# Performance work log

Hardware: AMD Instinct MI355X
Metric: run time of the kernel (lower is better)

The kernel has to match this reference:

```python
import jax, jax.numpy as jnp
import numpy as np

HEAD_SIZE = 64
N_EMBED = 1024

def setup_inputs() -> dict:
    key = jax.random.key(0)
    kx, kk, kq, kv = jax.random.split(key, 4)
    x = jax.random.normal(kx, (8, 2048, N_EMBED), dtype=jnp.float32)
    # torch nn.Linear weights: [out_features, in_features]
    s = 1.0 / np.sqrt(N_EMBED)
    Wk = jax.random.uniform(kk, (HEAD_SIZE, N_EMBED), jnp.float32, -s, s)
    Wq = jax.random.uniform(kq, (HEAD_SIZE, N_EMBED), jnp.float32, -s, s)
    Wv = jax.random.uniform(kv, (HEAD_SIZE, N_EMBED), jnp.float32, -s, s)
    return {"x": x, "Wk": Wk, "Wq": Wq, "Wv": Wv}

def reference(x, Wk, Wq, Wv):
    B, T, C = x.shape
    k = x @ Wk.T  # [B,T,H]
    q = x @ Wq.T
    v = x @ Wv.T
    # NOTE: original computes k @ q^T and scales by sqrt(C)=sqrt(n_embed)
    wei = jnp.einsum('btd,bsd->bts', k, q) / jnp.sqrt(jnp.float32(C))
    mask = jnp.tril(jnp.ones((T, T), dtype=bool))
    wei = jnp.where(mask, wei, -jnp.inf)
    wei = jax.nn.softmax(wei, axis=-1)
    return wei @ v  # [B,T,H]
```

## Files before the change

kernel.cpp:

```cpp
#include <hip/hip_runtime.h>
#include <hip/hip_bf16.h>


typedef __attribute__((ext_vector_type(8))) short short8;
typedef __attribute__((ext_vector_type(4))) float f32x4;
typedef __attribute__((ext_vector_type(16))) float f32x16;
typedef unsigned int u32;

#define BATCH 8
#define T 2048
#define CDIM 1024
#define HD 64
#define QK_SCALE 0.04508422f

static __device__ __forceinline__ short f2bf(float f) {
    return __builtin_bit_cast(short, __float2bfloat16(f));
}
static __device__ __forceinline__ float bf2f(unsigned short s) {
    u32 u = ((u32)s) << 16;
    return __builtin_bit_cast(float, u);
}
static __device__ __forceinline__ u32 packbf(float lo, float hi) {
    return (u32)(unsigned short)f2bf(lo) | ((u32)(unsigned short)f2bf(hi) << 16);
}
static __device__ __forceinline__ f32x4 mfma16(short8 a, short8 b, f32x4 c) {
    return __builtin_amdgcn_mfma_f32_16x16x32_bf16(a, b, c, 0, 0, 0);
}
static __device__ __forceinline__ f32x16 mfma32(short8 a, short8 b, f32x16 c) {
    return __builtin_amdgcn_mfma_f32_32x32x16_bf16(a, b, c, 0, 0, 0);
}

#define SOFT_BARRIER { \
    __builtin_amdgcn_sched_barrier(0); \
    asm volatile("s_waitcnt lgkmcnt(0)" ::: "memory"); \
    __builtin_amdgcn_s_barrier(); \
    __builtin_amdgcn_sched_barrier(0); }

__global__ __launch_bounds__(256) void wcvt_kernel(
    const float* __restrict__ Wk, const float* __restrict__ Wq,
    const float* __restrict__ Wv, short* __restrict__ wfrag)
{
    const int t = blockIdx.x * 256 + threadIdx.x;
    const int lane = t & 63, kk = (t >> 6) & 31, d16 = (t >> 11) & 3, p = t >> 13;
    const float* __restrict__ W = (p == 0) ? Wk : (p == 1 ? Wq : Wv);
    const float sc = (p == 0) ? QK_SCALE : 1.0f;
    const float* src = W + (size_t)(d16 * 16 + (lane & 15)) * CDIM
                         + kk * 32 + ((lane >> 4) & 3) * 8;
    f32x4 a = *(const f32x4*)src;
    f32x4 b = *(const f32x4*)(src + 4);
    short8 o;
#pragma unroll
    for (int e = 0; e < 4; ++e) { o[e] = f2bf(a[e] * sc); o[e + 4] = f2bf(b[e] * sc); }
    *(short8*)(wfrag + (size_t)t * 8) = o;
}

#define XLOAD(KC) { \
    xr0 = *(const f32x4*)(xsrc + (KC) * 64); \
    xr1 = *(const f32x4*)(xsrc + (KC) * 64 + 4); }

#define XWRITE(BASE) { \
    short8 v = { f2bf(xr0[0]), f2bf(xr0[1]), f2bf(xr0[2]), f2bf(xr0[3]), \
                 f2bf(xr1[0]), f2bf(xr1[1]), f2bf(xr1[2]), f2bf(xr1[3]) }; \
    *(short8*)((BASE) + srow * 128 + ((sseg * 16) ^ ((srow & 7) << 4))) = v; }

#define BLOAD(DST, KC) \
    _Pragma("unroll") for (int u = 0; u < 6; ++u) \
        DST[u] = *(const short8*)&wfrag[(size_t)((cg * 3 + (u % 3)) * 32 + (KC) * 2 + (u / 3)) * 512 + lane * 8];

#define COMPUTE(XBASE, B) \
    _Pragma("unroll") for (int kkL = 0; kkL < 2; ++kkL) { \
        short8 af0 = *(short8*)((XBASE) + c * 128 + ((kkL * 64 + g * 16) ^ ((c & 7) << 4))); \
        short8 af1 = *(short8*)((XBASE) + (16 + c) * 128 + ((kkL * 64 + g * 16) ^ ((c & 7) << 4))); \
        _Pragma("unroll") for (int j = 0; j < 3; ++j) { \
            acc[0][j] = mfma16(af0, B[kkL * 3 + j], acc[0][j]); \
            acc[1][j] = mfma16(af1, B[kkL * 3 + j], acc[1][j]); } }

__global__ __launch_bounds__(256) void proj_kernel(
    const float* __restrict__ x, const short* __restrict__ wfrag,
    short* __restrict__ kfrag, short* __restrict__ qfrag, short* __restrict__ vfrag)
{
    __shared__ __align__(16) char lds[16384];

    const int tid = threadIdx.x, cg = tid >> 6, lane = tid & 63;
    const int c = lane & 15, g = lane >> 4;
    const int srow = tid >> 3, sseg = tid & 7;
    const int row0 = blockIdx.x * 32;
    const float* __restrict__ xsrc = x + (size_t)(row0 + srow) * CDIM + sseg * 8;

    f32x4 acc[2][3] = {};
    short8 bC[6], bN[6];
    f32x4 xr0, xr1;

    XLOAD(0)
    XWRITE(lds)
    XLOAD(1)
    BLOAD(bC, 0)
    __syncthreads();

#pragma unroll
    for (int k = 0; k < 16; ++k) {
        char* pc = lds + (k % 3) * 4096;
        char* pw = lds + ((k + 1) % 3) * 4096;
        if (k < 15) { XWRITE(pw) }
        if (k < 14) { XLOAD(k + 2) }
        if (k < 15) { BLOAD(bN, k + 1) }
        COMPUTE(pc, bC)
        SOFT_BARRIER
        if (k < 15) {
#pragma unroll
            for (int u = 0; u < 6; ++u) bC[u] = bN[u];
        }
    }

    short* st_k = (short*)lds;
    short* st_q = (short*)(lds + 4608);
    short* st_v = (short*)(lds + 9216);
#pragma unroll
    for (int j = 0; j < 3; ++j) {
        const int q = cg * 3 + j, p = q >> 2, d16 = q & 3;
#pragma unroll
        for (int rh = 0; rh < 2; ++rh)
#pragma unroll
            for (int r = 0; r < 4; ++r) {
                const int mrow = rh * 16 + g * 4 + r;
                const short v = f2bf(acc[rh][j][r]);
                if (p == 0)      st_k[mrow * 72 + d16 * 16 + c] = v;
                else if (p == 1) st_q[mrow * 72 + d16 * 16 + c] = v;
                else             st_v[(d16 * 16 + c) * 40 + mrow] = v;
            }
    }
    __syncthreads();

    const int b = row0 >> 11, i = (row0 & 2047) >> 5;
    const size_t tb = ((size_t)(b * 64 + i)) * 4;
    const int l5 = lane & 31, h = lane >> 5;
    const int fq = cg;

    short8 kv = *(short8*)&st_k[l5 * 72 + fq * 16 + h * 8];
    *(short8*)&kfrag[(tb + fq) * 512 + lane * 8] = kv;
    short8 qv = *(short8*)&st_q[l5 * 72 + fq * 16 + h * 8];
    *(short8*)&qfrag[(tb + fq) * 512 + lane * 8] = qv;
    const int dh = fq >> 1, ssub = fq & 1;
    short8 vv = *(short8*)&st_v[(dh * 32 + l5) * 40 + ssub * 16 + h * 8];
    *(short8*)&vfrag[(tb + fq) * 512 + lane * 8] = vv;
}

__global__ __launch_bounds__(512) void attn_kernel(
    const short* __restrict__ kfrag, const short* __restrict__ qfrag,
    const short* __restrict__ vfrag, float* __restrict__ out)
{
    const int tid = threadIdx.x, wid = tid >> 6, lane = tid & 63;
    const int l5 = lane & 31, h = lane >> 5;
    const int bx = blockIdx.x;
    const int i = 63 - (bx >> 3);
    const int b = bx & 7;
    const int t0 = i * 32;

    __shared__ u32   sO[8][32][32];
    __shared__ float sML[8][2][32];

    const short* __restrict__ kb = kfrag + ((size_t)(b * 64 + i)) * 2048;
    const short* __restrict__ qb = qfrag + ((size_t)b * 64) * 2048;
    const short* __restrict__ vb = vfrag + ((size_t)b * 64) * 2048;

    short8 kf[4];
#pragma unroll
    for (int ks = 0; ks < 4; ++ks)
        kf[ks] = *(const short8*)&kb[ks * 512 + lane * 8];

    float m = -1e30f, l = 0.f;
    f32x16 o0 = {}, o1 = {};

    short8 qf[4], vf[4], qn[4], vn[4];
#pragma unroll
    for (int ks = 0; ks < 4; ++ks) {
        qf[ks] = *(const short8*)&qb[((size_t)wid * 4 + ks) * 512 + lane * 8];
        vf[ks] = *(const short8*)&vb[((size_t)wid * 4 + ks) * 512 + lane * 8];
    }

    for (int st = wid; st <= i; st += 8) {
        f32x16 Cs = {};
#pragma unroll
        for (int ks = 0; ks < 4; ++ks)
            Cs = mfma32(qf[ks], kf[ks], Cs);

        if (st + 8 <= i) {
#pragma unroll
            for (int ks = 0; ks < 4; ++ks) {
                qn[ks] = *(const short8*)&qb[((size_t)(st + 8) * 4 + ks) * 512 + lane * 8];
                vn[ks] = *(const short8*)&vb[((size_t)(st + 8) * 4 + ks) * 512 + lane * 8];
            }
        }

        if (st == i) {
#pragma unroll
            for (int r = 0; r < 16; ++r) {
                const int srow = (r & 3) + 8 * (r >> 2) + 4 * h;
                if (srow > l5) Cs[r] = -1e30f;
            }
        }
        float mx = fmaxf(Cs[0], Cs[1]);
#pragma unroll
        for (int r = 2; r < 16; ++r) mx = fmaxf(mx, Cs[r]);
        mx = fmaxf(mx, __shfl_xor(mx, 32));
        if (!__all(mx <= m)) {
            const float mnew = fmaxf(m, mx);
            const float alpha = exp2f(m - mnew);
            m = mnew;
            l *= alpha;
#pragma unroll
            for (int r = 0; r < 16; ++r) { o0[r] *= alpha; o1[r] *= alpha; }
        }
        u32 pk[8];
        float rs = 0.f;
#pragma unroll
        for (int q = 0; q < 8; ++q) {
            const float e0 = exp2f(Cs[2 * q] - m);
            const float e1 = exp2f(Cs[2 * q + 1] - m);
            rs += e0 + e1;
            pk[q] = packbf(e0, e1);
        }
        rs += __shfl_xor(rs, 32);
        l += rs;

        u32 w0 = pk[0], w2 = pk[2];
        asm volatile("v_permlane32_swap_b32 %0, %1" : "+v"(w0), "+v"(w2));
        u32 w1 = pk[1], w3 = pk[3];
        asm volatile("v_permlane32_swap_b32 %0, %1" : "+v"(w1), "+v"(w3));
        u32 w4 = pk[4], w6 = pk[6];
        asm volatile("v_permlane32_swap_b32 %0, %1" : "+v"(w4), "+v"(w6));
        u32 w5 = pk[5], w7 = pk[7];
        asm volatile("v_permlane32_swap_b32 %0, %1" : "+v"(w5), "+v"(w7));
        short8 pf0, pf1;
        pf0[0] = (short)(w0 & 0xffff); pf0[1] = (short)(w0 >> 16);
        pf0[2] = (short)(w1 & 0xffff); pf0[3] = (short)(w1 >> 16);
        pf0[4] = (short)(w2 & 0xffff); pf0[5] = (short)(w2 >> 16);
        pf0[6] = (short)(w3 & 0xffff); pf0[7] = (short)(w3 >> 16);
        pf1[0] = (short)(w4 & 0xffff); pf1[1] = (short)(w4 >> 16);
        pf1[2] = (short)(w5 & 0xffff); pf1[3] = (short)(w5 >> 16);
        pf1[4] = (short)(w6 & 0xffff); pf1[5] = (short)(w6 >> 16);
        pf1[6] = (short)(w7 & 0xffff); pf1[7] = (short)(w7 >> 16);

        o0 = mfma32(vf[0], pf0, o0);
        o0 = mfma32(vf[1], pf1, o0);
        o1 = mfma32(vf[2], pf0, o1);
        o1 = mfma32(vf[3], pf1, o1);

#pragma unroll
        for (int ks = 0; ks < 4; ++ks) { qf[ks] = qn[ks]; vf[ks] = vn[ks]; }
    }

#pragma unroll
    for (int q = 0; q < 8; ++q) {
        const int dp = (q & 1) + 4 * (q >> 1) + 2 * h;
        sO[wid][dp][l5]      = packbf(o0[2 * q], o0[2 * q + 1]);
        sO[wid][16 + dp][l5] = packbf(o1[2 * q], o1[2 * q + 1]);
    }
    if (h == 0) { sML[wid][0][l5] = m; sML[wid][1][l5] = l; }
    __syncthreads();

    float M = -1e30f;
#pragma unroll
    for (int p = 0; p < 8; ++p) M = fmaxf(M, sML[p][0][l5]);
    float L = 0.f;
    float av[4] = {};
#pragma unroll
    for (int p = 0; p < 8; ++p) {
        const float w = exp2f(sML[p][0][l5] - M);
        L += w * sML[p][1][l5];
#pragma unroll
        for (int dd2 = 0; dd2 < 2; ++dd2) {
            const u32 v = sO[p][wid * 4 + h * 2 + dd2][l5];
            av[2 * dd2]     += w * bf2f((unsigned short)(v & 0xffff));
            av[2 * dd2 + 1] += w * bf2f((unsigned short)(v >> 16));
        }
    }
    const float inv = 1.f / L;
    f32x4 r = { av[0] * inv, av[1] * inv, av[2] * inv, av[3] * inv };
    *(f32x4*)&out[((size_t)b * T + t0 + l5) * HD + wid * 8 + h * 4] = r;
}

extern "C" void kernel_launch(void* const* d_in, const int* in_sizes, int n_in,
                              void* d_out, int out_size, void* d_ws, size_t ws_size,
                              hipStream_t stream) {
    const float* x  = (const float*)d_in[0];
    const float* Wk = (const float*)d_in[1];
    const float* Wq = (const float*)d_in[2];
    const float* Wv = (const float*)d_in[3];
    float* out = (float*)d_out;

    short* kfrag = (short*)d_ws;
    short* qfrag = kfrag + (size_t)BATCH * T * HD;
    short* vfrag = qfrag + (size_t)BATCH * T * HD;
    short* wfrag = vfrag + (size_t)BATCH * T * HD;

    wcvt_kernel<<<96, 256, 0, stream>>>(Wk, Wq, Wv, wfrag);
    proj_kernel<<<512, 256, 0, stream>>>(x, wfrag, kfrag, qfrag, vfrag);
    attn_kernel<<<512, 512, 0, stream>>>(kfrag, qfrag, vfrag, out);
}
```

Baseline: 43.63 us.

## Give each wave a private double-buffered x tile to drop per-step block barriers

```diff
diff --git a/kernel.cpp b/kernel.cpp
--- a/kernel.cpp
+++ b/kernel.cpp
@@ -5,6 +5,7 @@
 typedef __attribute__((ext_vector_type(8))) short short8;
 typedef __attribute__((ext_vector_type(4))) float f32x4;
 typedef __attribute__((ext_vector_type(16))) float f32x16;
+typedef __attribute__((ext_vector_type(2))) unsigned int u32x2;
 typedef unsigned int u32;
 
 #define BATCH 8
@@ -29,12 +30,6 @@
 static __device__ __forceinline__ f32x16 mfma32(short8 a, short8 b, f32x16 c) {
     return __builtin_amdgcn_mfma_f32_32x32x16_bf16(a, b, c, 0, 0, 0);
 }
-
-#define SOFT_BARRIER { \
-    __builtin_amdgcn_sched_barrier(0); \
-    asm volatile("s_waitcnt lgkmcnt(0)" ::: "memory"); \
-    __builtin_amdgcn_s_barrier(); \
-    __builtin_amdgcn_sched_barrier(0); }
 
 __global__ __launch_bounds__(256) void wcvt_kernel(
     const float* __restrict__ Wk, const float* __restrict__ Wq,
@@ -54,14 +49,16 @@
     *(short8*)(wfrag + (size_t)t * 8) = o;
 }
 
-#define XLOAD(KC) { \
-    xr0 = *(const f32x4*)(xsrc + (KC) * 64); \
-    xr1 = *(const f32x4*)(xsrc + (KC) * 64 + 4); }
-
-#define XWRITE(BASE) { \
-    short8 v = { f2bf(xr0[0]), f2bf(xr0[1]), f2bf(xr0[2]), f2bf(xr0[3]), \
-                 f2bf(xr1[0]), f2bf(xr1[1]), f2bf(xr1[2]), f2bf(xr1[3]) }; \
-    *(short8*)((BASE) + srow * 128 + ((sseg * 16) ^ ((srow & 7) << 4))) = v; }
+#define XLOAD(KC) \
+    _Pragma("unroll") for (int u = 0; u < 8; ++u) \
+        xr[u] = *(const f32x4*)(xsrc + (size_t)((u >> 1) * 8) * CDIM + (KC) * 64 + (u & 1) * 32);
+
+#define XWRITE(BASE) \
+    _Pragma("unroll") for (int u = 0; u < 8; ++u) { \
+        const int rw = (u >> 1) * 8 + (lane >> 3); \
+        const int bo = (u & 1) * 64 + (lane & 7) * 8; \
+        u32x2 pv = { packbf(xr[u][0], xr[u][1]), packbf(xr[u][2], xr[u][3]) }; \
+        *(u32x2*)((BASE) + rw * 128 + (((bo & ~15) ^ ((rw & 7) << 4)) | (bo & 15))) = pv; }
 
 #define BLOAD(DST, KC) \
     _Pragma("unroll") for (int u = 0; u < 6; ++u) \
@@ -79,39 +76,38 @@
     const float* __restrict__ x, const short* __restrict__ wfrag,
     short* __restrict__ kfrag, short* __restrict__ qfrag, short* __restrict__ vfrag)
 {
-    __shared__ __align__(16) char lds[16384];
+    __shared__ __align__(16) char lds[32768];
 
     const int tid = threadIdx.x, cg = tid >> 6, lane = tid & 63;
     const int c = lane & 15, g = lane >> 4;
-    const int srow = tid >> 3, sseg = tid & 7;
     const int row0 = blockIdx.x * 32;
-    const float* __restrict__ xsrc = x + (size_t)(row0 + srow) * CDIM + sseg * 8;
+    char* myb = lds + cg * 8192;
+    const float* __restrict__ xsrc =
+        x + (size_t)(row0 + (lane >> 3)) * CDIM + (lane & 7) * 4;
 
     f32x4 acc[2][3] = {};
     short8 bC[6], bN[6];
-    f32x4 xr0, xr1;
+    f32x4 xr[8];
 
     XLOAD(0)
-    XWRITE(lds)
+    XWRITE(myb)
     XLOAD(1)
     BLOAD(bC, 0)
-    __syncthreads();
 
 #pragma unroll
     for (int k = 0; k < 16; ++k) {
-        char* pc = lds + (k % 3) * 4096;
-        char* pw = lds + ((k + 1) % 3) * 4096;
-        if (k < 15) { XWRITE(pw) }
+        char* pc = myb + (k & 1) * 4096;
+        if (k < 15) { XWRITE(myb + ((k + 1) & 1) * 4096) }
         if (k < 14) { XLOAD(k + 2) }
         if (k < 15) { BLOAD(bN, k + 1) }
         COMPUTE(pc, bC)
-        SOFT_BARRIER
         if (k < 15) {
 #pragma unroll
             for (int u = 0; u < 6; ++u) bC[u] = bN[u];
         }
     }
 
+    __syncthreads();
     short* st_k = (short*)lds;
     short* st_q = (short*)(lds + 4608);
     short* st_v = (short*)(lds + 9216);
```

After: 47.64 us. 1.09x slower.
